# Optimization experiments

Hardware: AMD Instinct MI355X
Metric: run time of the kernel (lower is better)

Reference implementation:

```python
import jax, jax.numpy as jnp
import numpy as np

N_COM = 100  # number of communities


def _gat(x, src, dst, ew, W, a_s, a_d):
    # Weighted multi-head GAT layer. x: [N,F], src/dst: [E], ew: [E]
    N = x.shape[0]
    H, dh = a_s.shape
    h = (x @ W).reshape(N, H, dh)              # [N,H,dh]
    hs, hd = h[src], h[dst]                     # [E,H,dh]
    e = jax.nn.leaky_relu((hs * a_s).sum(-1) + (hd * a_d).sum(-1), 0.2)  # [E,H]
    m = jax.ops.segment_max(e, dst, num_segments=N)  # [N,H] stable softmax max
    m = jnp.where(jnp.isfinite(m), m, 0.0)
    ex = jnp.exp(e - m[dst]) * ew[:, None]      # edge-weighted attention numerator
    den = jax.ops.segment_sum(ex, dst, num_segments=N)          # [N,H]
    num = jax.ops.segment_sum(ex[:, :, None] * hs, dst, num_segments=N)  # [N,H,dh]
    out = num / (den[:, :, None] + 1e-16)
    return jax.nn.elu(out.reshape(N, H * dh))


def _meso(x, part, D):
    # WeiPool_noW: degree-weighted mean pooling per community, scattered back to nodes
    num = jax.ops.segment_sum(D[:, None] * x, part, num_segments=N_COM)  # [C,d]
    den = jax.ops.segment_sum(D, part, num_segments=N_COM)               # [C]
    mean = num / (den[:, None] + 1e-16)
    return mean[part]                                                     # [N,d]


def _lstm_cell(h, c, x, Wx, Wh, b):
    z = x @ Wx + h @ Wh + b
    i, f, g, o = jnp.split(z, 4, axis=-1)
    c = jax.nn.sigmoid(f) * c + jax.nn.sigmoid(i) * jnp.tanh(g)
    h = jax.nn.sigmoid(o) * jnp.tanh(c)
    return h, c


def setup_inputs() -> dict:
    key = jax.random.key(0)
    ks = jax.random.split(key, 20)
    T, N, E, F = 8, 10000, 320000, 128
    H = 4
    d1, d2 = 128, 64            # micro_dims[1], micro_dims[2]
    d_rnn = 128                 # RNN_dims[1]; RNN input = 2*d2 = 128
    d_dec = 64                  # decoder_dims[1]
    s = 0.05
    inp = {
        'feat': jax.random.normal(ks[0], (T, N, F), jnp.float32),
        'edge_weight': jax.random.uniform(ks[1], (T, E), jnp.float32),
        'D': jax.random.uniform(ks[2], (T, N), jnp.float32),
        'W1': jax.random.normal(ks[3], (F, d1), jnp.float32) * s,
        'a_src1': jax.random.normal(ks[4], (H, d1 // H), jnp.float32) * s,
        'a_dst1': jax.random.normal(ks[5], (H, d1 // H), jnp.float32) * s,
        'W2': jax.random.normal(ks[6], (d1, d2), jnp.float32) * s,
        'a_src2': jax.random.normal(ks[7], (H, d2 // H), jnp.float32) * s,
        'a_dst2': jax.random.normal(ks[8], (H, d2 // H), jnp.float32) * s,
        'Wx': jax.random.normal(ks[9], (2 * d2, 4 * d_rnn), jnp.float32) * s,
        'Wh': jax.random.normal(ks[10], (d_rnn, 4 * d_rnn), jnp.float32) * s,
        'b_lstm': jnp.zeros((4 * d_rnn,), jnp.float32),
        'emb_W': jax.random.normal(ks[11], (d_rnn, d_dec), jnp.float32) * s,
        'emb_b': jnp.zeros((d_dec,), jnp.float32),
        'scal_W': jax.random.normal(ks[12], (d_rnn, d_dec), jnp.float32) * s,
        'scal_b': jnp.zeros((d_dec,), jnp.float32),
        'edge_index': jax.random.randint(ks[13], (T, 2, E), 0, N, jnp.int64),
        'partition': jax.random.randint(ks[14], (T, N), 0, N_COM, jnp.int64),
    }
    return inp


def reference(feat, edge_weight, D, W1, a_src1, a_dst1, W2, a_src2, a_dst2,
              Wx, Wh, b_lstm, emb_W, emb_b, scal_W, scal_b,
              edge_index, partition):
    T, N, _ = feat.shape
    src, dst = edge_index[:, 0], edge_index[:, 1]          # [T,E]
    gat = jax.vmap(_gat, in_axes=(0, 0, 0, 0, None, None, None))
    g1 = gat(feat, src, dst, edge_weight, W1, a_src1, a_dst1)   # [T,N,d1]
    g2 = gat(g1, src, dst, edge_weight, W2, a_src2, a_dst2)     # [T,N,d2]
    meso = jax.vmap(_meso)(g2, partition, D)                    # [T,N,d2]
    agg = jnp.concatenate([g2, meso], axis=-1)                  # [T,N,2*d2]

    d_h = Wh.shape[0]
    h0 = jnp.zeros((N, d_h), feat.dtype)

    def step(carry, x):
        h, c = carry
        h, c = _lstm_cell(h, c, x, Wx, Wh, b_lstm)
        return (h, c), h

    _, hs = jax.lax.scan(step, (h0, h0), agg)                   # [T,N,d_h]
    h_last = hs[-1]

    emb = jnp.tanh(h_last @ emb_W + emb_b)                      # decoder emb path
    emb = emb / jnp.linalg.norm(emb, axis=0, keepdims=True)     # F.normalize dim=0
    scal = jax.nn.sigmoid(h_last @ scal_W + scal_b)             # decoder scal path
    S = scal @ scal.T                                            # [N,N]
    G = emb @ emb.T
    sq = jnp.diag(G)
    dist = -(sq[:, None] + sq[None, :] - 2.0 * G)                # -||e_i - e_j||^2
    adj_est = 1.0 + jnp.tanh(dist * S)
    return adj_est
```

## Files before the change

### kernel.cpp

```cpp
#include <hip/hip_runtime.h>
#include <cstddef>
#include <cstdint>

#define T_   8
#define N_   10000
#define E_   320000
#define F_   128
#define D1_  128
#define D2_  64
#define DR_  128
#define NC_  100
#define TN_  (T_*N_)
#define TE_  (T_*E_)
#define NPAD_ 10112

typedef __attribute__((ext_vector_type(8))) short bf16x8;
typedef __attribute__((ext_vector_type(8))) ushort u16x8;
typedef __attribute__((ext_vector_type(4))) float f32x4;

__device__ __forceinline__ float bf2f(ushort u) {
    return __uint_as_float(((unsigned int)u) << 16);
}
__device__ __forceinline__ ushort f2bf(float f) {
    unsigned int u = __float_as_uint(f);
    unsigned int r = (u + 0x7FFFu + ((u >> 16) & 1u)) >> 16;
    return (ushort)r;
}
__device__ __forceinline__ float fast_tanh(float x) {
    float t = __expf(2.f * x);
    return 1.f - 2.f / (t + 1.f);
}
__device__ __forceinline__ float fast_sigmoid(float x) {
    return 1.f / (1.f + __expf(-x));
}

__global__ __launch_bounds__(256) void conv_feat(const float* __restrict__ src,
                                                 ushort* __restrict__ dst, int n8)
{
    int idx = blockIdx.x * 256 + threadIdx.x;
    if (idx >= n8) return;
    const float4* s = (const float4*)src + (size_t)idx * 2;
    float4 x = s[0], y = s[1];
    u16x8 o;
    o[0]=f2bf(x.x); o[1]=f2bf(x.y); o[2]=f2bf(x.z); o[3]=f2bf(x.w);
    o[4]=f2bf(y.x); o[5]=f2bf(y.y); o[6]=f2bf(y.z); o[7]=f2bf(y.w);
    *((u16x8*)dst + idx) = o;
}

__global__ __launch_bounds__(256) void conv_weights(
    const float* __restrict__ W1, const float* __restrict__ W2,
    const float* __restrict__ Wx, const float* __restrict__ Wh,
    const float* __restrict__ eW, const float* __restrict__ sW,
    ushort* __restrict__ W1T, ushort* __restrict__ W2T,
    ushort* __restrict__ WxT, ushort* __restrict__ WhT,
    ushort* __restrict__ eWT, ushort* __restrict__ sWT)
{
    int idx = blockIdx.x * 256 + threadIdx.x;
    if (idx < 16384)       { int n=idx>>7,   k=idx&127;            W1T[idx]=f2bf(W1[k*128+n]); }
    else if (idx < 24576)  { int l=idx-16384;  int n=l>>7,k=l&127; W2T[l]=f2bf(W2[k*64+n]); }
    else if (idx < 90112)  { int l=idx-24576;  int n=l>>7,k=l&127; WxT[l]=f2bf(Wx[k*512+n]); }
    else if (idx < 155648) { int l=idx-90112;  int n=l>>7,k=l&127; WhT[l]=f2bf(Wh[k*512+n]); }
    else if (idx < 163840) { int l=idx-155648; int n=l>>7,k=l&127; eWT[l]=f2bf(eW[k*64+n]); }
    else if (idx < 172032) { int l=idx-163840; int n=l>>7,k=l&127; sWT[l]=f2bf(sW[k*64+n]); }
}

__global__ __launch_bounds__(256) void gemm_bf16(
    const ushort* __restrict__ A, const ushort* __restrict__ BT,
    float* __restrict__ Cf, ushort* __restrict__ Cb,
    const float* __restrict__ bias, const float* __restrict__ addsrc,
    int M, int K, int Nc, int act)
{
    int w = threadIdx.x >> 6, lane = threadIdx.x & 63;
    int quad = lane >> 4, l16 = lane & 15;
    int m0 = blockIdx.y * 128 + w * 32;
    int n0 = blockIdx.x * 64;
    f32x4 zf = {0.f, 0.f, 0.f, 0.f};
    f32x4 acc[2][4];
    #pragma unroll
    for (int rt = 0; rt < 2; ++rt)
        #pragma unroll
        for (int ct = 0; ct < 4; ++ct) acc[rt][ct] = zf;

    for (int k0 = 0; k0 < K; k0 += 32) {
        int kk = k0 + quad * 8;
        bf16x8 a0 = *(const bf16x8*)(A + (size_t)(m0 + l16) * K + kk);
        bf16x8 a1 = *(const bf16x8*)(A + (size_t)(m0 + 16 + l16) * K + kk);
        bf16x8 b[4];
        #pragma unroll
        for (int ct = 0; ct < 4; ++ct)
            b[ct] = *(const bf16x8*)(BT + (size_t)(n0 + ct * 16 + l16) * K + kk);
        #pragma unroll
        for (int ct = 0; ct < 4; ++ct) {
            acc[0][ct] = __builtin_amdgcn_mfma_f32_16x16x32_bf16(a0, b[ct], acc[0][ct], 0, 0, 0);
            acc[1][ct] = __builtin_amdgcn_mfma_f32_16x16x32_bf16(a1, b[ct], acc[1][ct], 0, 0, 0);
        }
    }

    #pragma unroll
    for (int rt = 0; rt < 2; ++rt) {
        int ibase = m0 + rt * 16 + quad * 4;
        #pragma unroll
        for (int r = 0; r < 4; ++r) {
            int i = ibase + r;
            if (i >= M) continue;
            #pragma unroll
            for (int ct = 0; ct < 4; ++ct) {
                int j = n0 + ct * 16 + l16;
                float v = acc[rt][ct][r];
                if (bias)   v += bias[j];
                if (addsrc) v += addsrc[(size_t)i * Nc + j];
                if (act == 1)      v = fast_tanh(v);
                else if (act == 2) v = fast_sigmoid(v);
                if (Cf) Cf[(size_t)i * Nc + j] = v;
                if (Cb) Cb[(size_t)i * Nc + j] = f2bf(v);
            }
        }
    }
}

__global__ __launch_bounds__(256) void att_vec128(
    const ushort* __restrict__ h, const float* __restrict__ a_src,
    const float* __restrict__ a_dst, float* __restrict__ as_out,
    float* __restrict__ ad_out, int rows)
{
    int wid  = (blockIdx.x * 256 + threadIdx.x) >> 6;
    int lane = threadIdx.x & 63;
    if (wid >= rows) return;
    const ushort* hr = h + (size_t)wid * 128;
    float v0 = bf2f(hr[lane]), v1 = bf2f(hr[64 + lane]);
    float pa0 = v0 * a_src[lane], pa1 = v1 * a_src[64 + lane];
    float pd0 = v0 * a_dst[lane], pd1 = v1 * a_dst[64 + lane];
    #pragma unroll
    for (int m = 1; m <= 16; m <<= 1) {
        pa0 += __shfl_xor(pa0, m); pa1 += __shfl_xor(pa1, m);
        pd0 += __shfl_xor(pd0, m); pd1 += __shfl_xor(pd1, m);
    }
    if ((lane & 31) == 0) {
        int g = lane >> 5;
        as_out[wid * 4 + g] = pa0; as_out[wid * 4 + 2 + g] = pa1;
        ad_out[wid * 4 + g] = pd0; ad_out[wid * 4 + 2 + g] = pd1;
    }
}

__global__ __launch_bounds__(256) void att_vec64(
    const ushort* __restrict__ h, const float* __restrict__ a_src,
    const float* __restrict__ a_dst, float* __restrict__ as_out,
    float* __restrict__ ad_out, int rows)
{
    int wid  = (blockIdx.x * 256 + threadIdx.x) >> 6;
    int lane = threadIdx.x & 63;
    if (wid >= rows) return;
    float v = bf2f(h[(size_t)wid * 64 + lane]);
    float pa = v * a_src[lane], pd = v * a_dst[lane];
    #pragma unroll
    for (int m = 1; m <= 8; m <<= 1) { pa += __shfl_xor(pa, m); pd += __shfl_xor(pd, m); }
    if ((lane & 15) == 0) {
        int g = lane >> 4;
        as_out[wid * 4 + g] = pa; ad_out[wid * 4 + g] = pd;
    }
}

__global__ void count_edges(const int* __restrict__ eidx, int* __restrict__ counts)
{
    int idx = blockIdx.x * 256 + threadIdx.x;
    if (idx >= TE_) return;
    int t = idx / E_, e = idx - t * E_;
    int d = eidx[(size_t)t * 2 * E_ + E_ + e];
    atomicAdd(&counts[t * N_ + d], 1);
}

__global__ __launch_bounds__(1024) void scan_per_t(
    const int* __restrict__ counts, int* __restrict__ rowptr, int* __restrict__ cursor)
{
    const int CH = 10;
    int t = blockIdx.x, i = threadIdx.x;
    int base0 = t * N_;
    int cnt[CH];
    int s = 0;
    int g0 = i * CH;
    #pragma unroll
    for (int q = 0; q < CH; ++q) {
        int g = g0 + q;
        cnt[q] = (g < N_) ? counts[base0 + g] : 0;
        s += cnt[q];
    }
    __shared__ int buf[1024];
    buf[i] = s;
    __syncthreads();
    for (int off = 1; off < 1024; off <<= 1) {
        int v = (i >= off) ? buf[i - off] : 0;
        __syncthreads();
        buf[i] += v;
        __syncthreads();
    }
    int run = t * E_ + buf[i] - s;
    #pragma unroll
    for (int q = 0; q < CH; ++q) {
        int g = g0 + q;
        if (g < N_) {
            rowptr[base0 + g] = run;
            cursor[base0 + g] = run;
            run += cnt[q];
        }
    }
    if (t == T_ - 1 && i == 1023) rowptr[T_ * N_] = TE_;
}

__global__ void fill_csr(const int* __restrict__ eidx, const float* __restrict__ ew,
                         int* __restrict__ cursor, int* __restrict__ src_csr,
                         float* __restrict__ ew_csr)
{
    int idx = blockIdx.x * 256 + threadIdx.x;
    if (idx >= TE_) return;
    int t = idx / E_, e = idx - t * E_;
    int s = eidx[(size_t)t * 2 * E_ + e];
    int d = eidx[(size_t)t * 2 * E_ + E_ + e];
    float w = ew[(size_t)t * E_ + e];
    int pos = atomicAdd(&cursor[t * N_ + d], 1);
    src_csr[pos] = t * N_ + s;
    ew_csr[pos] = w;
}

__global__ __launch_bounds__(256) void gat_node_128(
    const ushort* __restrict__ h, const float* __restrict__ as,
    const float* __restrict__ ad, const int* __restrict__ rowptr,
    const int* __restrict__ src_csr, const float* __restrict__ ew_csr,
    ushort* __restrict__ outp, int rows)
{
    int wid  = (blockIdx.x * 256 + threadIdx.x) >> 6;
    int lane = threadIdx.x & 63;
    if (wid >= rows) return;
    int start = rowptr[wid], end = rowptr[wid + 1];
    int h0 = lane >> 5, h1 = 2 + h0;
    float ad0 = ad[wid * 4 + h0], ad1 = ad[wid * 4 + h1];
    float acc0 = 0.f, acc1 = 0.f, den0 = 0.f, den1 = 0.f;
    for (int p = start; p < end; ++p) {
        int s = src_csr[p];
        float w = ew_csr[p];
        float e0 = as[s * 4 + h0] + ad0; e0 = e0 > 0.f ? e0 : 0.2f * e0;
        float e1 = as[s * 4 + h1] + ad1; e1 = e1 > 0.f ? e1 : 0.2f * e1;
        float x0 = __expf(e0) * w;
        float x1 = __expf(e1) * w;
        den0 += x0; den1 += x1;
        const ushort* hs = h + (size_t)s * 128;
        acc0 += x0 * bf2f(hs[lane]);
        acc1 += x1 * bf2f(hs[64 + lane]);
    }
    float o0 = acc0 / (den0 + 1e-16f);
    float o1 = acc1 / (den1 + 1e-16f);
    o0 = o0 > 0.f ? o0 : (__expf(o0) - 1.f);
    o1 = o1 > 0.f ? o1 : (__expf(o1) - 1.f);
    outp[(size_t)wid * 128 + lane]      = f2bf(o0);
    outp[(size_t)wid * 128 + 64 + lane] = f2bf(o1);
}

__global__ __launch_bounds__(256) void gat_node_64(
    const ushort* __restrict__ h, const float* __restrict__ as,
    const float* __restrict__ ad, const int* __restrict__ rowptr,
    const int* __restrict__ src_csr, const float* __restrict__ ew_csr,
    ushort* __restrict__ outp, int rows)
{
    int wid  = (blockIdx.x * 256 + threadIdx.x) >> 6;
    int lane = threadIdx.x & 63;
    if (wid >= rows) return;
    int start = rowptr[wid], end = rowptr[wid + 1];
    int hh = lane >> 4;
    float adv = ad[wid * 4 + hh];
    float acc = 0.f, den = 0.f;
    for (int p = start; p < end; ++p) {
        int s = src_csr[p];
        float w = ew_csr[p];
        float e = as[s * 4 + hh] + adv; e = e > 0.f ? e : 0.2f * e;
        float x = __expf(e) * w;
        den += x;
        acc += x * bf2f(h[(size_t)s * 64 + lane]);
    }
    float o = acc / (den + 1e-16f);
    o = o > 0.f ? o : (__expf(o) - 1.f);
    outp[(size_t)wid * 64 + lane] = f2bf(o);
}

__global__ __launch_bounds__(256) void meso_acc(
    const ushort* __restrict__ g2, const int* __restrict__ part,
    const float* __restrict__ Dw, float* __restrict__ msum, float* __restrict__ mden)
{
    int wid  = (blockIdx.x * 256 + threadIdx.x) >> 6;
    int lane = threadIdx.x & 63;
    if (wid >= TN_) return;
    int t = wid / N_;
    int p = part[wid];
    float dv = Dw[wid];
    atomicAdd(&msum[((size_t)(t * NC_ + p) << 6) + lane], dv * bf2f(g2[(size_t)wid * 64 + lane]));
    if (lane == 0) atomicAdd(&mden[t * NC_ + p], dv);
}

__global__ void agg_assemble(
    const ushort* __restrict__ g2, const int* __restrict__ part,
    const float* __restrict__ msum, const float* __restrict__ mden,
    ushort* __restrict__ agg)
{
    int idx = blockIdx.x * 256 + threadIdx.x;
    int row = idx >> 7, d = idx & 127;
    ushort v;
    if (d < 64) {
        v = g2[(size_t)row * 64 + d];
    } else {
        int t = row / N_;
        int p = part[row];
        v = f2bf(msum[((size_t)(t * NC_ + p) << 6) + (d - 64)] / (mden[t * NC_ + p] + 1e-16f));
    }
    agg[idx] = v;
}

__global__ void lstm_cell(const float* __restrict__ z, float* __restrict__ c,
                          ushort* __restrict__ hb)
{
    int idx = blockIdx.x * 256 + threadIdx.x;
    int n = idx >> 7, j = idx & 127;
    const float* zr = z + (size_t)n * 512;
    float zi = zr[j], zf = zr[128 + j], zg = zr[256 + j], zo = zr[384 + j];
    float si = fast_sigmoid(zi);
    float sf = fast_sigmoid(zf);
    float so = fast_sigmoid(zo);
    float cn = sf * c[idx] + si * fast_tanh(zg);
    c[idx] = cn;
    hb[(size_t)n * 128 + j] = f2bf(so * fast_tanh(cn));
}

__global__ __launch_bounds__(256) void col_sumsq(const float* __restrict__ emb,
                                                 float* __restrict__ colss)
{
    int tid = threadIdx.x;
    int col = tid & 63, rq = tid >> 6;
    float s = 0.f;
    for (int r = blockIdx.x * 4 + rq; r < N_; r += 40 * 4) {
        float v = emb[(size_t)r * 64 + col];
        s += v * v;
    }
    __shared__ float red[256];
    red[tid] = s;
    __syncthreads();
    if (tid < 64)
        atomicAdd(&colss[tid], red[tid] + red[tid + 64] + red[tid + 128] + red[tid + 192]);
}

__global__ __launch_bounds__(256) void norm_rows(const float* __restrict__ emb,
                                                 const float* __restrict__ colss,
                                                 ushort* __restrict__ embb,
                                                 float* __restrict__ sq, int rows)
{
    int wid  = (blockIdx.x * 256 + threadIdx.x) >> 6;
    int lane = threadIdx.x & 63;
    if (wid >= rows) return;
    float nv = emb[(size_t)wid * 64 + lane] / sqrtf(colss[lane]);
    ushort ub = f2bf(nv);
    embb[(size_t)wid * 64 + lane] = ub;
    float nq = bf2f(ub);
    float q = nq * nq;
    #pragma unroll
    for (int m = 1; m <= 32; m <<= 1) q += __shfl_xor(q, m);
    if (lane == 0) sq[wid] = q;
}

__global__ __launch_bounds__(256) void final_adj_mfma(
    const ushort* __restrict__ embb, const ushort* __restrict__ scalb,
    const float* __restrict__ sq, float* __restrict__ outp)
{
    int w = threadIdx.x >> 6, lane = threadIdx.x & 63;
    int quad = lane >> 4, l16 = lane & 15;
    int bi = blockIdx.y * 128 + (w >> 1) * 64;
    int bj = blockIdx.x * 128 + (w & 1) * 64;
    f32x4 zf = {0.f, 0.f, 0.f, 0.f};
    f32x4 accS[4][4], accG[4][4];
    #pragma unroll
    for (int rt = 0; rt < 4; ++rt)
        #pragma unroll
        for (int ct = 0; ct < 4; ++ct) { accS[rt][ct] = zf; accG[rt][ct] = zf; }

    #pragma unroll
    for (int ks = 0; ks < 2; ++ks) {
        int k0 = ks * 32 + quad * 8;
        bf16x8 ae[4], af[4], be[4], bs[4];
        #pragma unroll
        for (int t = 0; t < 4; ++t) {
            int ri = bi + t * 16 + l16;
            int rj = bj + t * 16 + l16;
            ae[t] = *(const bf16x8*)(embb  + (size_t)ri * 64 + k0);
            af[t] = *(const bf16x8*)(scalb + (size_t)ri * 64 + k0);
            be[t] = *(const bf16x8*)(embb  + (size_t)rj * 64 + k0);
            bs[t] = *(const bf16x8*)(scalb + (size_t)rj * 64 + k0);
        }
        #pragma unroll
        for (int rt = 0; rt < 4; ++rt)
            #pragma unroll
            for (int ct = 0; ct < 4; ++ct) {
                accG[rt][ct] = __builtin_amdgcn_mfma_f32_16x16x32_bf16(be[ct], ae[rt], accG[rt][ct], 0, 0, 0);
                accS[rt][ct] = __builtin_amdgcn_mfma_f32_16x16x32_bf16(bs[ct], af[rt], accS[rt][ct], 0, 0, 0);
            }
    }

    #pragma unroll
    for (int rt = 0; rt < 4; ++rt) {
        int i = bi + rt * 16 + l16;
        if (i >= N_) continue;
        float sqi = sq[i];
        #pragma unroll
        for (int ct = 0; ct < 4; ++ct) {
            int j0 = bj + ct * 16 + quad * 4;
            if (j0 >= N_) continue;
            const float4 sj = *(const float4*)(sq + j0);
            float sjr[4] = { sj.x, sj.y, sj.z, sj.w };
            f32x4 v;
            #pragma unroll
            for (int r = 0; r < 4; ++r) {
                float G = accG[rt][ct][r], S = accS[rt][ct][r];
                float dist = 2.f * G - sqi - sjr[r];
                float t = __expf(2.f * dist * S);
                v[r] = 2.f - 2.f / (t + 1.f);
            }
            __builtin_nontemporal_store(v, (f32x4*)(outp + (size_t)i * N_ + j0));
        }
    }
}

extern "C" void kernel_launch(void* const* d_in, const int* in_sizes, int n_in,
                              void* d_out, int out_size, void* d_ws, size_t ws_size,
                              hipStream_t stream)
{
    (void)in_sizes; (void)n_in; (void)out_size; (void)ws_size;
    const float* feat    = (const float*)d_in[0];
    const float* eweight = (const float*)d_in[1];
    const float* Dw      = (const float*)d_in[2];
    const float* W1      = (const float*)d_in[3];
    const float* a_src1  = (const float*)d_in[4];
    const float* a_dst1  = (const float*)d_in[5];
    const float* W2      = (const float*)d_in[6];
    const float* a_src2  = (const float*)d_in[7];
    const float* a_dst2  = (const float*)d_in[8];
    const float* Wx      = (const float*)d_in[9];
    const float* Wh      = (const float*)d_in[10];
    const float* b_lstm  = (const float*)d_in[11];
    const float* emb_W   = (const float*)d_in[12];
    const float* emb_b   = (const float*)d_in[13];
    const float* scal_W  = (const float*)d_in[14];
    const float* scal_b  = (const float*)d_in[15];
    const int*   eidx    = (const int*)d_in[16];
    const int*   part    = (const int*)d_in[17];

    float* out = (float*)d_out;
    ushort* h1b   = (ushort*)(out + 0);
    ushort* g1b   = (ushort*)(out + 5120000);
    ushort* h2b   = (ushort*)(out + 10240000);
    ushort* g2b   = (ushort*)(out + 12800000);
    float* as1    = out + 15360000;
    float* ad1    = out + 15680000;
    float* as2    = out + 16000000;
    float* ad2    = out + 16320000;
    int*   rowptr = (int*)(out + 16640000);
    int*   cursor = (int*)(out + 16720064);
    int*   counts = (int*)(out + 16800064);
    int*   src_csr= (int*)(out + 16880064);
    float* ew_csr = out + 19440064;
    float* msum   = out + 22000064;
    float* mden   = out + 22051264;
    ushort* aggb  = (ushort*)(out + 22052064);
    float* ZX     = out + 27172064;
    float* zbuf   = out + 68132064;
    float* cstate = out + 73252064;
    ushort* hbf   = (ushort*)(out + 74532064);
    ushort* featb = (ushort*)(out + 75179232);
    ushort* W1T   = (ushort*)(out + 80299232);
    ushort* W2T   = (ushort*)(out + 80307424);
    ushort* WxT   = (ushort*)(out + 80311520);
    ushort* WhT   = (ushort*)(out + 80344288);
    ushort* eWT   = (ushort*)(out + 80377056);
    ushort* sWT   = (ushort*)(out + 80381152);
    float* embf   = out + 80385248;
    float* colss  = out + 81025248;

    ushort* embb  = (ushort*)d_ws;
    ushort* scalb = embb + (size_t)NPAD_ * 64;
    float*  sq    = (float*)(scalb + (size_t)NPAD_ * 64);

    hipMemsetAsync(counts, 0, TN_ * sizeof(int), stream);
    hipMemsetAsync(msum, 0, (T_ * NC_ * 64 + T_ * NC_) * sizeof(float), stream);
    hipMemsetAsync(cstate, 0, (size_t)N_ * DR_ * sizeof(float), stream);
    hipMemsetAsync(hbf, 0, (size_t)NPAD_ * DR_ * sizeof(ushort), stream);
    hipMemsetAsync(colss, 0, 64 * sizeof(float), stream);

    conv_feat<<<5000, 256, 0, stream>>>(feat, featb, TN_ * F_ / 8);
    conv_weights<<<672, 256, 0, stream>>>(W1, W2, Wx, Wh, emb_W, scal_W,
                                          W1T, W2T, WxT, WhT, eWT, sWT);

    gemm_bf16<<<dim3(2, 625), 256, 0, stream>>>(featb, W1T, nullptr, h1b, nullptr, nullptr, TN_, 128, 128, 0);
    att_vec128<<<TN_/4, 256, 0, stream>>>(h1b, a_src1, a_dst1, as1, ad1, TN_);
    count_edges<<<(TE_+255)/256, 256, 0, stream>>>(eidx, counts);
    scan_per_t<<<T_, 1024, 0, stream>>>(counts, rowptr, cursor);
    fill_csr<<<(TE_+255)/256, 256, 0, stream>>>(eidx, eweight, cursor, src_csr, ew_csr);
    gat_node_128<<<TN_/4, 256, 0, stream>>>(h1b, as1, ad1, rowptr, src_csr, ew_csr, g1b, TN_);

    gemm_bf16<<<dim3(1, 625), 256, 0, stream>>>(g1b, W2T, nullptr, h2b, nullptr, nullptr, TN_, 128, 64, 0);
    att_vec64<<<TN_/4, 256, 0, stream>>>(h2b, a_src2, a_dst2, as2, ad2, TN_);
    gat_node_64<<<TN_/4, 256, 0, stream>>>(h2b, as2, ad2, rowptr, src_csr, ew_csr, g2b, TN_);

    meso_acc<<<TN_/4, 256, 0, stream>>>(g2b, part, Dw, msum, mden);
    agg_assemble<<<TN_*128/256, 256, 0, stream>>>(g2b, part, msum, mden, aggb);

    gemm_bf16<<<dim3(8, 625), 256, 0, stream>>>(aggb, WxT, ZX, nullptr, b_lstm, nullptr, TN_, 128, 512, 0);
    for (int t = 0; t < T_; ++t) {
        gemm_bf16<<<dim3(8, 79), 256, 0, stream>>>(hbf, WhT, zbuf, nullptr, nullptr,
                                                   ZX + (size_t)t * N_ * 512, N_, 128, 512, 0);
        lstm_cell<<<N_*DR_/256, 256, 0, stream>>>(zbuf, cstate, hbf);
    }

    gemm_bf16<<<dim3(1, 79), 256, 0, stream>>>(hbf, eWT, embf, nullptr, emb_b, nullptr, N_, 128, 64, 1);
    gemm_bf16<<<dim3(1, 79), 256, 0, stream>>>(hbf, sWT, nullptr, scalb, scal_b, nullptr, N_, 128, 64, 2);
    col_sumsq<<<40, 256, 0, stream>>>(embf, colss);
    norm_rows<<<(N_+3)/4, 256, 0, stream>>>(embf, colss, embb, sq, N_);

    final_adj_mfma<<<dim3(79, 79), 256, 0, stream>>>(embb, scalb, sq, out);
}
```

Measured before the change: 1.952 ms.

## Stage final adjacency tiles in LDS for aligned coalesced row stores

The final N×N adjacency kernel now walks five 128-column tiles per block and stages each computed tile in shared memory. Rows are then written with full-width, 16-byte aligned nontemporal stores. Because N is 10000, odd rows start at an address 16 bytes off a 64-byte boundary, so odd rows are written with a 16-column shift and a carry buffer holds the previous tile's edge. The aim is to improve write coalescing and alignment on the 400 MB output, which dominates runtime, at the cost of extra LDS traffic, two barriers per tile and fewer blocks.

```diff
diff --git a/kernel.cpp b/kernel.cpp
--- a/kernel.cpp
+++ b/kernel.cpp
@@ -362,63 +362,123 @@
     if (lane == 0) sq[wid] = q;
 }
 
+#define FTJ_   5
+#define FCOLS_ (FTJ_*128)
+
 __global__ __launch_bounds__(256) void final_adj_mfma(
     const ushort* __restrict__ embb, const ushort* __restrict__ scalb,
     const float* __restrict__ sq, float* __restrict__ outp)
 {
+    __shared__ float cur[128][132];
+    __shared__ float edg[2][64][16];
+
     int w = threadIdx.x >> 6, lane = threadIdx.x & 63;
     int quad = lane >> 4, l16 = lane & 15;
-    int bi = blockIdx.y * 128 + (w >> 1) * 64;
-    int bj = blockIdx.x * 128 + (w & 1) * 64;
-    f32x4 zf = {0.f, 0.f, 0.f, 0.f};
-    f32x4 accS[4][4], accG[4][4];
-    #pragma unroll
-    for (int rt = 0; rt < 4; ++rt)
-        #pragma unroll
-        for (int ct = 0; ct < 4; ++ct) { accS[rt][ct] = zf; accG[rt][ct] = zf; }
-
-    #pragma unroll
-    for (int ks = 0; ks < 2; ++ks) {
-        int k0 = ks * 32 + quad * 8;
-        bf16x8 ae[4], af[4], be[4], bs[4];
-        #pragma unroll
-        for (int t = 0; t < 4; ++t) {
-            int ri = bi + t * 16 + l16;
-            int rj = bj + t * 16 + l16;
-            ae[t] = *(const bf16x8*)(embb  + (size_t)ri * 64 + k0);
-            af[t] = *(const bf16x8*)(scalb + (size_t)ri * 64 + k0);
-            be[t] = *(const bf16x8*)(embb  + (size_t)rj * 64 + k0);
-            bs[t] = *(const bf16x8*)(scalb + (size_t)rj * 64 + k0);
-        }
+    int bi = blockIdx.y * 128;
+    int Wb = blockIdx.x * FCOLS_;
+    int wi = bi + (w >> 1) * 64;
+
+    float sqi[4];
+    #pragma unroll
+    for (int rt = 0; rt < 4; ++rt) sqi[rt] = sq[wi + rt * 16 + l16];
+
+    int tLast = (N_ - 1 - Wb) / 128;
+    if (tLast > FTJ_ - 1) tLast = FTJ_ - 1;
+
+    for (int t = 0; t <= tLast; ++t) {
+        int Wt = Wb + t * 128;
+        int wj = Wt + (w & 1) * 64;
+
+        f32x4 zf = {0.f, 0.f, 0.f, 0.f};
+        f32x4 accG[4][4], accS[4][4];
         #pragma unroll
         for (int rt = 0; rt < 4; ++rt)
             #pragma unroll
+            for (int ct = 0; ct < 4; ++ct) { accG[rt][ct] = zf; accS[rt][ct] = zf; }
+
+        #pragma unroll
+        for (int ks = 0; ks < 2; ++ks) {
+            int k0 = ks * 32 + quad * 8;
+            bf16x8 ae[4], af[4], be[4], bs[4];
+            #pragma unroll
+            for (int q = 0; q < 4; ++q) {
+                int ri = wi + q * 16 + l16;
+                int rj = wj + q * 16 + l16;
+                ae[q] = *(const bf16x8*)(embb  + (size_t)ri * 64 + k0);
+                af[q] = *(const bf16x8*)(scalb + (size_t)ri * 64 + k0);
+                be[q] = *(const bf16x8*)(embb  + (size_t)rj * 64 + k0);
+                bs[q] = *(const bf16x8*)(scalb + (size_t)rj * 64 + k0);
+            }
+            #pragma unroll
+            for (int rt = 0; rt < 4; ++rt)
+                #pragma unroll
+                for (int ct = 0; ct < 4; ++ct) {
+                    accG[rt][ct] = __builtin_amdgcn_mfma_f32_16x16x32_bf16(be[ct], ae[rt], accG[rt][ct], 0, 0, 0);
+                    accS[rt][ct] = __builtin_amdgcn_mfma_f32_16x16x32_bf16(bs[ct], af[rt], accS[rt][ct], 0, 0, 0);
+                }
+        }
+
+        __syncthreads();
+
+        #pragma unroll
+        for (int rt = 0; rt < 4; ++rt) {
+            int li = (w >> 1) * 64 + rt * 16 + l16;
+            float si = sqi[rt];
+            #pragma unroll
             for (int ct = 0; ct < 4; ++ct) {
-                accG[rt][ct] = __builtin_amdgcn_mfma_f32_16x16x32_bf16(be[ct], ae[rt], accG[rt][ct], 0, 0, 0);
-                accS[rt][ct] = __builtin_amdgcn_mfma_f32_16x16x32_bf16(bs[ct], af[rt], accS[rt][ct], 0, 0, 0);
+                int lj = (w & 1) * 64 + ct * 16 + quad * 4;
+                const float4 sj = *(const float4*)(sq + Wt + lj);
+                float sjr[4] = { sj.x, sj.y, sj.z, sj.w };
+                f32x4 v;
+                #pragma unroll
+                for (int r = 0; r < 4; ++r) {
+                    float G = accG[rt][ct][r], S = accS[rt][ct][r];
+                    float dist = 2.f * G - si - sjr[r];
+                    float e = __expf(2.f * dist * S);
+                    v[r] = 2.f - 2.f / (e + 1.f);
+                }
+                *(f32x4*)&cur[li][lj] = v;
+                if ((w & 1) && ct == 3 && (li & 1))
+                    *(f32x4*)&edg[t & 1][li >> 1][quad * 4] = v;
             }
-    }
-
-    #pragma unroll
-    for (int rt = 0; rt < 4; ++rt) {
-        int i = bi + rt * 16 + l16;
-        if (i >= N_) continue;
-        float sqi = sq[i];
-        #pragma unroll
-        for (int ct = 0; ct < 4; ++ct) {
-            int j0 = bj + ct * 16 + quad * 4;
-            if (j0 >= N_) continue;
-            const float4 sj = *(const float4*)(sq + j0);
-            float sjr[4] = { sj.x, sj.y, sj.z, sj.w };
-            f32x4 v;
-            #pragma unroll
-            for (int r = 0; r < 4; ++r) {
-                float G = accG[rt][ct][r], S = accS[rt][ct][r];
-                float dist = 2.f * G - sqi - sjr[r];
-                float t = __expf(2.f * dist * S);
-                v[r] = 2.f - 2.f / (t + 1.f);
+        }
+
+        __syncthreads();
+
+        int lane5 = lane & 31;
+        #pragma unroll
+        for (int pass = 0; pass < 16; ++pass) {
+            int r = pass * 8 + (lane >> 5) * 4 + w;
+            int i = bi + r;
+            if (i < N_) {
+                if (!(r & 1)) {
+                    int gcol = Wt + lane5 * 4;
+                    if (gcol < N_)
+                        __builtin_nontemporal_store(*(const f32x4*)&cur[r][lane5 * 4],
+                            (f32x4*)(outp + (size_t)i * N_ + gcol));
+                } else {
+                    int gcol = Wt - 16 + lane5 * 4;
+                    if ((t > 0 || lane5 >= 4) && gcol >= 0 && gcol < N_) {
+                        f32x4 v;
+                        if (lane5 < 4) v = *(const f32x4*)&edg[(t & 1) ^ 1][r >> 1][lane5 * 4];
+                        else           v = *(const f32x4*)&cur[r][lane5 * 4 - 16];
+                        __builtin_nontemporal_store(v,
+                            (f32x4*)(outp + (size_t)i * N_ + gcol));
+                    }
+                }
             }
-            __builtin_nontemporal_store(v, (f32x4*)(outp + (size_t)i * N_ + j0));
+        }
+    }
+
+    {
+        int tid = threadIdx.x;
+        int r = ((tid >> 2) << 1) | 1;
+        int k = (tid & 3) * 4;
+        int i = bi + r;
+        int gcol = Wb + tLast * 128 + 112 + k;
+        if (i < N_ && gcol < N_) {
+            f32x4 v = *(const f32x4*)&cur[r][112 + k];
+            __builtin_nontemporal_store(v, (f32x4*)(outp + (size_t)i * N_ + gcol));
         }
     }
 }
@@ -518,5 +578,5 @@
     col_sumsq<<<40, 256, 0, stream>>>(embf, colss);
     norm_rows<<<(N_+3)/4, 256, 0, stream>>>(embf, colss, embb, sq, N_);
 
-    final_adj_mfma<<<dim3(79, 79), 256, 0, stream>>>(embb, scalb, sq, out);
-}
+    final_adj_mfma<<<dim3(16, 79), 256, 0, stream>>>(embb, scalb, sq, out);
+}
```

New measurement: 1.870 ms. 4.2% less time.
